# Kernel optimization log

Hardware: AMD Instinct MI355X
Metric: run time of the kernel (lower is better)

## Reference

```python
import jax, jax.numpy as jnp
import numpy as np

D_MODEL = 1024
N_TILES = 16
BATCH = 32768
THRESH = 0.3


def setup_inputs() -> dict:
    key = jax.random.key(0)
    k_x, k_sig, k_w, k_b = jax.random.split(key, 4)
    x = jax.random.normal(k_x, (BATCH, D_MODEL), dtype=jnp.float32)
    # nn.Parameter(torch.randn(n_tiles, d_model) * 0.5)
    signatures_raw = jax.random.normal(k_sig, (N_TILES, D_MODEL), dtype=jnp.float32) * 0.5
    # nn.Linear(d_model, d_model) default init: U(-1/sqrt(fan_in), 1/sqrt(fan_in))
    bound = 1.0 / np.sqrt(D_MODEL)
    W = jax.random.uniform(k_w, (N_TILES, D_MODEL, D_MODEL), dtype=jnp.float32, minval=-bound, maxval=bound)
    b = jax.random.uniform(k_b, (N_TILES, D_MODEL), dtype=jnp.float32, minval=-bound, maxval=bound)
    return {"x": x, "signatures_raw": signatures_raw, "W": W, "b": b}


def _quantize_ternary(s):
    # straight-through ternary: forward value is q, gradient is identity
    q = jnp.where(s > THRESH, 1.0, jnp.where(s < -THRESH, -1.0, 0.0))
    return s + jax.lax.stop_gradient(q - s)


def reference(x, signatures_raw, W, b):
    sigs = _quantize_ternary(signatures_raw)          # [E, D]
    scores = x @ sigs.T                               # [B, E]
    tile_indices = jnp.argmax(scores, axis=-1)        # [B]
    out = jnp.zeros_like(x)
    # fixed small loop over experts: masked combine of per-expert Linear+ReLU
    for e in range(N_TILES):
        y = jax.nn.relu(x @ W[e].T + b[e])            # [B, D]
        out = out + jnp.where((tile_indices == e)[:, None], y, 0.0)
    out = out + x                                     # residual
    return out, tile_indices
```

## Files before the change

### kernel.cpp

```cpp
#include <hip/hip_runtime.h>
#include <hip/hip_bf16.h>

#define BATCH   32768
#define DM      1024
#define NE      16
#define THRESHF 0.3f
#define MARGIN  0.02f

#define CTRL_OFF 131072
#define QBF_OFF  139264
#define PERM_OFF 172032
#define XBF_OFF  319488
#define WB_OFF   67428352ull
#define WS_NEED  (WB_OFF + (size_t)NE * DM * DM * 2)

typedef __attribute__((ext_vector_type(8))) short bf16x8;
typedef __attribute__((ext_vector_type(4))) float f32x4;

#define MFMA16(a, b, c) __builtin_amdgcn_mfma_f32_16x16x32_bf16(a, b, c, 0, 0, 0)

static __device__ __forceinline__ unsigned short f2bf(float f) {
    union { float f; unsigned u; } v; v.f = f;
    unsigned r = (v.u + 0x7FFFu + ((v.u >> 16) & 1u)) >> 16;
    return (unsigned short)r;
}
static __device__ __forceinline__ float bf2f(unsigned short h) {
    union { unsigned u; float f; } v; v.u = ((unsigned)h) << 16;
    return v.f;
}

static __device__ __forceinline__ void gload_lds16(const void* g, void* s) {
    __builtin_amdgcn_global_load_lds(
        (const __attribute__((address_space(1))) void*)g,
        (__attribute__((address_space(3))) void*)s, 16, 0, 0);
}

static __device__ __forceinline__ int tile_base(const unsigned* ctrl, int* tb) {
    int acc = 0;
#pragma unroll
    for (int e = 0; e < NE; ++e) {
        tb[e] = acc;
        acc += (int)((ctrl[e * 16] + 127u) >> 7);
    }
    tb[NE] = acc;
    return acc;
}

__global__ void k_init(const float* __restrict__ sig, unsigned* __restrict__ ctrl,
                       int* __restrict__ perm, unsigned short* __restrict__ Qbf) {
    const int t = blockIdx.x * 256 + threadIdx.x;
    if (t < 544) ctrl[t] = 0;
    if (t < 1024) {
        unsigned pm = 0, mm = 0;
#pragma unroll
        for (int e = 0; e < NE; ++e) {
            float s = sig[e * DM + t];
            pm |= (s > THRESHF ? 1u : 0u) << e;
            mm |= (s < -THRESHF ? 1u : 0u) << e;
        }
        ctrl[1024 + t] = pm | (mm << 16);
    }
    if (t < 9216) ((int4*)perm)[t] = make_int4(0, 0, 0, 0);
    {
        float s = sig[t];
        Qbf[t] = s > THRESHF ? (unsigned short)0x3F80u
                             : (s < -THRESHF ? (unsigned short)0xBF80u : (unsigned short)0u);
    }
}

__global__ __launch_bounds__(256) void k_router(const float* __restrict__ x,
                                                const unsigned short* __restrict__ Qbf,
                                                unsigned* __restrict__ ctrl,
                                                int* __restrict__ idx,
                                                float* __restrict__ outIdx,
                                                unsigned short* __restrict__ Xbf,
                                                int writeXbf) {
    const int t = threadIdx.x, w = t >> 6, l = t & 63;
    const int lc = l & 15, lr = l >> 4;
    const int wid = blockIdx.x * 4 + w;
    const int row0 = wid * 16;
    const unsigned* packT = ctrl + 1024;

    const float* ax = x + (size_t)(row0 + lc) * DM + lr * 8;
    const unsigned short* qx = Qbf + (size_t)lc * DM + lr * 8;
    unsigned short* xb = Xbf + (size_t)(row0 + lc) * DM + lr * 8;

    f32x4 acc = (f32x4){0.f, 0.f, 0.f, 0.f};

    for (int kt = 0; kt < 16; ++kt) {
#pragma unroll
        for (int h = 0; h < 2; ++h) {
            const int ko = kt * 64 + h * 32;
            float4 v0 = *(const float4*)(ax + ko);
            float4 v1 = *(const float4*)(ax + ko + 4);
            bf16x8 q = *(const bf16x8*)(qx + ko);

            float f[8] = {v0.x, v0.y, v0.z, v0.w, v1.x, v1.y, v1.z, v1.w};
            bf16x8 ah, al;
#pragma unroll
            for (int j = 0; j < 8; ++j) {
                unsigned short hi = f2bf(f[j]);
                float r = f[j] - bf2f(hi);
                ah[j] = (short)hi;
                al[j] = (short)f2bf(r);
            }
            if (writeXbf) *(bf16x8*)(xb + ko) = ah;
            acc = MFMA16(ah, q, acc);
            acc = MFMA16(al, q, acc);
        }
    }

    float bv[4]; int bi[4]; float gap[4];
#pragma unroll
    for (int reg = 0; reg < 4; ++reg) {
        float v = acc[reg]; int i = lc; float s = -3.4e38f;
#pragma unroll
        for (int m = 1; m < 16; m <<= 1) {
            float ov = __shfl_xor(v, m, 64);
            int oi = __shfl_xor(i, m, 64);
            float os = __shfl_xor(s, m, 64);
            bool take = (ov > v) || (ov == v && oi < i);
            float loser = take ? v : ov;
            v = take ? ov : v;
            i = take ? oi : i;
            s = fmaxf(fmaxf(s, os), loser);
        }
        bv[reg] = v; bi[reg] = i; gap[reg] = v - s;
    }

    unsigned flagsw = 0;
#pragma unroll
    for (int reg = 0; reg < 4; ++reg)
        flagsw |= (gap[reg] < MARGIN ? 1u : 0u) << reg;

    if (__any(lc == 0 && flagsw != 0)) {
#pragma unroll
        for (int reg = 0; reg < 4; ++reg) {
            for (int g = 0; g < 4; ++g) {
                const unsigned fw = __shfl(flagsw, g * 16, 64);
                if ((fw >> reg) & 1u) {
                    const int row = row0 + g * 4 + reg;
                    const float* xr = x + (size_t)row * DM;
                    float xv[16]; unsigned mk[16];
#pragma unroll
                    for (int k2 = 0; k2 < 16; ++k2) {
                        xv[k2] = xr[k2 * 64 + l];
                        mk[k2] = packT[k2 * 64 + l];
                    }
                    double best = 0.0; int bbi = 0;
                    for (int e = 0; e < 16; ++e) {
                        double a = 0.0;
#pragma unroll
                        for (int k2 = 0; k2 < 16; ++k2) {
                            const int pb = (int)((mk[k2] >> e) & 1u);
                            const int mb = (int)((mk[k2] >> (16 + e)) & 1u);
                            a += pb ? (double)xv[k2] : (mb ? -(double)xv[k2] : 0.0);
                        }
#pragma unroll
                        for (int m = 1; m < 64; m <<= 1) a += __shfl_xor(a, m, 64);
                        if (e == 0 || a > best) { best = a; bbi = e; }
                    }
                    if (lr == g && lc == 0) bi[reg] = bbi;
                }
            }
        }
    }

    if (lc == 0) {
#pragma unroll
        for (int reg = 0; reg < 4; ++reg) {
            const int row = row0 + lr * 4 + reg;
            idx[row] = bi[reg];
            outIdx[row] = (float)bi[reg];
            atomicAdd(&ctrl[bi[reg] * 16], 1u);
        }
    }
}

__global__ __launch_bounds__(256) void k_permconv(const int* __restrict__ idx,
                                                  unsigned* __restrict__ ctrl,
                                                  int* __restrict__ perm,
                                                  const float* __restrict__ W,
                                                  unsigned short* __restrict__ Wb) {
    if (blockIdx.x >= 128) {
        const size_t g = ((size_t)(blockIdx.x - 128) * 256 + threadIdx.x) * 8;
        float4 a = *(const float4*)&W[g];
        float4 b = *(const float4*)&W[g + 4];
        *(ushort4*)&Wb[g]     = make_ushort4(f2bf(a.x), f2bf(a.y), f2bf(a.z), f2bf(a.w));
        *(ushort4*)&Wb[g + 4] = make_ushort4(f2bf(b.x), f2bf(b.y), f2bf(b.z), f2bf(b.w));
        return;
    }
    __shared__ unsigned hcnt[16];
    __shared__ unsigned hbase[16];
    const int t = threadIdx.x;
    const int row = blockIdx.x * 256 + t;
    int tb[NE + 1];
    tile_base(ctrl, tb);
    if (t < 16) hcnt[t] = 0;
    __syncthreads();
    const int e = idx[row];
    const unsigned lrank = atomicAdd(&hcnt[e], 1u);
    __syncthreads();
    if (t < 16) hbase[t] = atomicAdd(&ctrl[256 + t * 16], hcnt[t]);
    __syncthreads();
    perm[tb[e] * 128 + hbase[e] + lrank] = row;
}

__global__ __launch_bounds__(256, 4) void k_gemm(
        const unsigned short* __restrict__ Xbf,
        const unsigned short* __restrict__ Wb,
        const float* __restrict__ bias,
        const int* __restrict__ perm,
        const unsigned* __restrict__ ctrl,
        float* __restrict__ out) {
    __shared__ unsigned short A_lds[3][128 * 32];
    __shared__ unsigned short B_lds[2][128 * 32];

    int tb[NE + 1];
    const int total = tile_base(ctrl, tb);

    int bx, ny;
    {
        const int flat = blockIdx.x;
        const int xcd = flat & 7, s2 = flat >> 3;
        bx = xcd * 34 + (s2 >> 3);
        ny = s2 & 7;
    }
    if (bx >= total) return;
    int e = 0;
    while (e < NE - 1 && tb[e + 1] <= bx) ++e;
    const int valid = (int)ctrl[e * 16] - (bx - tb[e]) * 128;
    const int n0 = ny * 128;

    const int t = threadIdx.x, w = t >> 6, l = t & 63;
    const int wr = w >> 1, wc = w & 1;
    const int lc = l & 15, lr = l >> 4;
    const int hsw = ((t & 3) - ((t >> 3) & 3)) & 3;
    const int ssw = (lr + (lc >> 1)) & 3;

    f32x4 acc[4][4];
#pragma unroll
    for (int m = 0; m < 4; ++m)
#pragma unroll
        for (int n = 0; n < 4; ++n) acc[m][n] = (f32x4){0.f, 0.f, 0.f, 0.f};

    const size_t aRowBase = (size_t)bx * 128;
    const unsigned short* Bg = Wb + ((size_t)e * DM + n0) * DM;

    const int r0 = t >> 2;
    const int prow0 = perm[aRowBase + r0];
    const int prow1 = perm[aRowBase + 64 + r0];
    const unsigned short* a0 = Xbf + (size_t)prow0 * DM + hsw * 8;
    const unsigned short* a1 = Xbf + (size_t)prow1 * DM + hsw * 8;
    const unsigned short* b0 = Bg + (size_t)(t >> 2) * DM + hsw * 8;
    const unsigned short* b1 = Bg + (size_t)(64 + (t >> 2)) * DM + hsw * 8;

    auto STAGE_A = [&](int kt, int buf) {
        const int ko = kt * 32;
        gload_lds16(a0 + ko, &A_lds[buf][(size_t)(w * 64) * 8]);
        gload_lds16(a1 + ko, &A_lds[buf][(size_t)(256 + w * 64) * 8]);
    };
    auto STAGE_B = [&](int kt, int buf) {
        const int ko = kt * 32;
        gload_lds16(b0 + ko, &B_lds[buf][(size_t)(w * 64) * 8]);
        gload_lds16(b1 + ko, &B_lds[buf][(size_t)(256 + w * 64) * 8]);
    };

    STAGE_A(0, 0);
    STAGE_B(0, 0);
    STAGE_A(1, 1);

    const int NT = DM / 32;
    for (int kt = 0; kt < NT; ++kt) {
        if (kt + 1 < NT) asm volatile("s_waitcnt vmcnt(2)" ::: "memory");
        else             asm volatile("s_waitcnt vmcnt(0)" ::: "memory");
        __builtin_amdgcn_sched_barrier(0);
        __builtin_amdgcn_s_barrier();
        __builtin_amdgcn_sched_barrier(0);

        const int ba = kt % 3, bb = kt & 1;
        if (kt + 1 < NT) STAGE_B(kt + 1, bb ^ 1);
        if (kt + 2 < NT) STAGE_A(kt + 2, (ba + 2 >= 3) ? ba - 1 : ba + 2);

        bf16x8 af[4], bf[4];
#pragma unroll
        for (int m = 0; m < 4; ++m)
            af[m] = *(const bf16x8*)&A_lds[ba][(wr * 64 + m * 16 + lc) * 32 + ssw * 8];
#pragma unroll
        for (int n = 0; n < 4; ++n)
            bf[n] = *(const bf16x8*)&B_lds[bb][(wc * 64 + n * 16 + lc) * 32 + ssw * 8];
#pragma unroll
        for (int m = 0; m < 4; ++m)
#pragma unroll
            for (int n = 0; n < 4; ++n)
                acc[m][n] = MFMA16(af[m], bf[n], acc[m][n]);
    }

    float bvv[4];
#pragma unroll
    for (int n = 0; n < 4; ++n) bvv[n] = bias[e * DM + n0 + wc * 64 + n * 16 + lc];

#pragma unroll
    for (int m = 0; m < 4; ++m) {
#pragma unroll
        for (int reg = 0; reg < 4; ++reg) {
            const int rit = wr * 64 + m * 16 + lr * 4 + reg;
            if (rit < valid) {
                const int orow = perm[aRowBase + rit];
                float* op = out + (size_t)orow * DM;
                const unsigned short* xr = Xbf + (size_t)orow * DM;
#pragma unroll
                for (int n = 0; n < 4; ++n) {
                    const int col = n0 + wc * 64 + n * 16 + lc;
                    float v = acc[m][n][reg] + bvv[n];
                    v = v > 0.f ? v : 0.f;
                    op[col] = v + bf2f(xr[col]);
                }
            }
        }
    }
}

__global__ __launch_bounds__(256) void k_gemm_small(
        const float* __restrict__ x, const float* __restrict__ W,
        const float* __restrict__ bias, const int* __restrict__ perm,
        const unsigned* __restrict__ ctrl, float* __restrict__ out) {
    __shared__ unsigned short A_lds[128 * 32];
    __shared__ unsigned short B_lds[128 * 32];
    int tb[NE + 1];
    const int total = tile_base(ctrl, tb);
    int bx, ny;
    {
        const int flat = blockIdx.x;
        const int xcd = flat & 7, s2 = flat >> 3;
        bx = xcd * 34 + (s2 >> 3);
        ny = s2 & 7;
    }
    if (bx >= total) return;
    int e = 0;
    while (e < NE - 1 && tb[e + 1] <= bx) ++e;
    const int valid = (int)ctrl[e * 16] - (bx - tb[e]) * 128;
    const int n0 = ny * 128;
    const int t = threadIdx.x, w = t >> 6, l = t & 63;
    const int wr = w >> 1, wc = w & 1;
    const int lc = l & 15, lr = l >> 4;
    const int hsw = ((t & 3) - ((t >> 3) & 3)) & 3;
    const int ssw = (lr + (lc >> 1)) & 3;

    f32x4 acc[4][4];
#pragma unroll
    for (int m = 0; m < 4; ++m)
#pragma unroll
        for (int n = 0; n < 4; ++n) acc[m][n] = (f32x4){0.f, 0.f, 0.f, 0.f};
    const size_t aRowBase = (size_t)bx * 128;

    for (int kt = 0; kt < DM / 32; ++kt) {
        __syncthreads();
#pragma unroll
        for (int rd = 0; rd < 2; ++rd) {
            const int c = rd * 256 + t;
            const int r = c >> 2;
            const float* wp = W + ((size_t)e * DM + n0 + r) * DM + kt * 32 + hsw * 8;
            float4 q0 = *(const float4*)wp;
            float4 q1 = *(const float4*)(wp + 4);
            *(ushort4*)&B_lds[c * 8]     = make_ushort4(f2bf(q0.x), f2bf(q0.y), f2bf(q0.z), f2bf(q0.w));
            *(ushort4*)&B_lds[c * 8 + 4] = make_ushort4(f2bf(q1.x), f2bf(q1.y), f2bf(q1.z), f2bf(q1.w));
            ushort4 p0 = make_ushort4(0, 0, 0, 0), p1 = p0;
            if (r < valid) {
                const int orow = perm[aRowBase + r];
                const float* xp = x + (size_t)orow * DM + kt * 32 + hsw * 8;
                float4 u0 = *(const float4*)xp;
                float4 u1 = *(const float4*)(xp + 4);
                p0 = make_ushort4(f2bf(u0.x), f2bf(u0.y), f2bf(u0.z), f2bf(u0.w));
                p1 = make_ushort4(f2bf(u1.x), f2bf(u1.y), f2bf(u1.z), f2bf(u1.w));
            }
            *(ushort4*)&A_lds[c * 8]     = p0;
            *(ushort4*)&A_lds[c * 8 + 4] = p1;
        }
        __syncthreads();
        bf16x8 af[4], bf[4];
#pragma unroll
        for (int m = 0; m < 4; ++m)
            af[m] = *(const bf16x8*)&A_lds[(wr * 64 + m * 16 + lc) * 32 + ssw * 8];
#pragma unroll
        for (int n = 0; n < 4; ++n)
            bf[n] = *(const bf16x8*)&B_lds[(wc * 64 + n * 16 + lc) * 32 + ssw * 8];
#pragma unroll
        for (int m = 0; m < 4; ++m)
#pragma unroll
            for (int n = 0; n < 4; ++n)
                acc[m][n] = MFMA16(af[m], bf[n], acc[m][n]);
    }

    float bvv[4];
#pragma unroll
    for (int n = 0; n < 4; ++n) bvv[n] = bias[e * DM + n0 + wc * 64 + n * 16 + lc];
#pragma unroll
    for (int m = 0; m < 4; ++m)
#pragma unroll
        for (int reg = 0; reg < 4; ++reg) {
            const int rit = wr * 64 + m * 16 + lr * 4 + reg;
            if (rit < valid) {
                const int orow = perm[aRowBase + rit];
                const float* xr = x + (size_t)orow * DM;
                float* op = out + (size_t)orow * DM;
#pragma unroll
                for (int n = 0; n < 4; ++n) {
                    const int col = n0 + wc * 64 + n * 16 + lc;
                    float v = acc[m][n][reg] + bvv[n];
                    v = v > 0.f ? v : 0.f;
                    op[col] = v + xr[col];
                }
            }
        }
}

extern "C" void kernel_launch(void* const* d_in, const int* in_sizes, int n_in,
                              void* d_out, int out_size, void* d_ws, size_t ws_size,
                              hipStream_t stream) {
    const float* x    = (const float*)d_in[0];
    const float* sig  = (const float*)d_in[1];
    const float* W    = (const float*)d_in[2];
    const float* bias = (const float*)d_in[3];
    float* out = (float*)d_out;
    float* outIdx = out + (size_t)BATCH * DM;

    char* ws = (char*)d_ws;
    int* idx = (int*)ws;
    unsigned* ctrl = (unsigned*)(ws + CTRL_OFF);
    unsigned short* Qbf = (unsigned short*)(ws + QBF_OFF);
    int* perm = (int*)(ws + PERM_OFF);
    unsigned short* Xbf = (unsigned short*)(ws + XBF_OFF);
    unsigned short* Wb = (unsigned short*)(ws + WB_OFF);

    const bool full = ws_size >= WS_NEED;

    k_init<<<64, 256, 0, stream>>>(sig, ctrl, perm, Qbf);
    k_router<<<512, 256, 0, stream>>>(x, Qbf, ctrl, idx, outIdx, Xbf, full ? 1 : 0);
    k_permconv<<<full ? 8320 : 128, 256, 0, stream>>>(idx, ctrl, perm, W, Wb);
    if (full) {
        k_gemm<<<2176, 256, 0, stream>>>(Xbf, Wb, bias, perm, ctrl, out);
    } else {
        k_gemm_small<<<2176, 256, 0, stream>>>(x, W, bias, perm, ctrl, out);
    }
}
```

Measured before the change: 255.3 us.

## Fuse W conversion into router kernel and triple-buffer B tiles in GEMM

The weight fp32-to-bf16 conversion moves from the permutation kernel into the router kernel as extra blocks, so the bandwidth-bound conversion runs alongside routing and the permutation kernel becomes small. In the GEMM, B is now triple-buffered like A, with one combined stage issuing both loads two iterations ahead and waiting on vmcnt(4). The occupancy hint in launch_bounds is dropped. More LDS per block may lower occupancy, and the router grid is now much larger.

```diff
diff --git a/kernel.cpp b/kernel.cpp
--- a/kernel.cpp
+++ b/kernel.cpp
@@ -68,13 +68,25 @@
     }
 }
 
-__global__ __launch_bounds__(256) void k_router(const float* __restrict__ x,
-                                                const unsigned short* __restrict__ Qbf,
-                                                unsigned* __restrict__ ctrl,
-                                                int* __restrict__ idx,
-                                                float* __restrict__ outIdx,
-                                                unsigned short* __restrict__ Xbf,
-                                                int writeXbf) {
+__global__ __launch_bounds__(256) void k_router_conv(
+        const float* __restrict__ x,
+        const unsigned short* __restrict__ Qbf,
+        unsigned* __restrict__ ctrl,
+        int* __restrict__ idx,
+        float* __restrict__ outIdx,
+        unsigned short* __restrict__ Xbf,
+        const float* __restrict__ W,
+        unsigned short* __restrict__ Wb,
+        int writeXbf) {
+    if (blockIdx.x >= 512) {
+        const size_t g = ((size_t)(blockIdx.x - 512) * 256 + threadIdx.x) * 8;
+        float4 a = *(const float4*)&W[g];
+        float4 b = *(const float4*)&W[g + 4];
+        *(ushort4*)&Wb[g]     = make_ushort4(f2bf(a.x), f2bf(a.y), f2bf(a.z), f2bf(a.w));
+        *(ushort4*)&Wb[g + 4] = make_ushort4(f2bf(b.x), f2bf(b.y), f2bf(b.z), f2bf(b.w));
+        return;
+    }
+
     const int t = threadIdx.x, w = t >> 6, l = t & 63;
     const int lc = l & 15, lr = l >> 4;
     const int wid = blockIdx.x * 4 + w;
@@ -177,19 +189,9 @@
     }
 }
 
-__global__ __launch_bounds__(256) void k_permconv(const int* __restrict__ idx,
-                                                  unsigned* __restrict__ ctrl,
-                                                  int* __restrict__ perm,
-                                                  const float* __restrict__ W,
-                                                  unsigned short* __restrict__ Wb) {
-    if (blockIdx.x >= 128) {
-        const size_t g = ((size_t)(blockIdx.x - 128) * 256 + threadIdx.x) * 8;
-        float4 a = *(const float4*)&W[g];
-        float4 b = *(const float4*)&W[g + 4];
-        *(ushort4*)&Wb[g]     = make_ushort4(f2bf(a.x), f2bf(a.y), f2bf(a.z), f2bf(a.w));
-        *(ushort4*)&Wb[g + 4] = make_ushort4(f2bf(b.x), f2bf(b.y), f2bf(b.z), f2bf(b.w));
-        return;
-    }
+__global__ __launch_bounds__(256) void k_perm(const int* __restrict__ idx,
+                                              unsigned* __restrict__ ctrl,
+                                              int* __restrict__ perm) {
     __shared__ unsigned hcnt[16];
     __shared__ unsigned hbase[16];
     const int t = threadIdx.x;
@@ -206,7 +208,7 @@
     perm[tb[e] * 128 + hbase[e] + lrank] = row;
 }
 
-__global__ __launch_bounds__(256, 4) void k_gemm(
+__global__ __launch_bounds__(256) void k_gemm(
         const unsigned short* __restrict__ Xbf,
         const unsigned short* __restrict__ Wb,
         const float* __restrict__ bias,
@@ -214,7 +216,7 @@
         const unsigned* __restrict__ ctrl,
         float* __restrict__ out) {
     __shared__ unsigned short A_lds[3][128 * 32];
-    __shared__ unsigned short B_lds[2][128 * 32];
+    __shared__ unsigned short B_lds[3][128 * 32];
 
     int tb[NE + 1];
     const int total = tile_base(ctrl, tb);
@@ -255,45 +257,45 @@
     const unsigned short* b0 = Bg + (size_t)(t >> 2) * DM + hsw * 8;
     const unsigned short* b1 = Bg + (size_t)(64 + (t >> 2)) * DM + hsw * 8;
 
-    auto STAGE_A = [&](int kt, int buf) {
+    auto STAGE = [&](int kt, int buf) {
         const int ko = kt * 32;
         gload_lds16(a0 + ko, &A_lds[buf][(size_t)(w * 64) * 8]);
         gload_lds16(a1 + ko, &A_lds[buf][(size_t)(256 + w * 64) * 8]);
-    };
-    auto STAGE_B = [&](int kt, int buf) {
-        const int ko = kt * 32;
         gload_lds16(b0 + ko, &B_lds[buf][(size_t)(w * 64) * 8]);
         gload_lds16(b1 + ko, &B_lds[buf][(size_t)(256 + w * 64) * 8]);
     };
 
-    STAGE_A(0, 0);
-    STAGE_B(0, 0);
-    STAGE_A(1, 1);
+    STAGE(0, 0);
+    STAGE(1, 1);
 
     const int NT = DM / 32;
+    int cur = 0;
     for (int kt = 0; kt < NT; ++kt) {
-        if (kt + 1 < NT) asm volatile("s_waitcnt vmcnt(2)" ::: "memory");
+        if (kt + 1 < NT) asm volatile("s_waitcnt vmcnt(4)" ::: "memory");
         else             asm volatile("s_waitcnt vmcnt(0)" ::: "memory");
         __builtin_amdgcn_sched_barrier(0);
         __builtin_amdgcn_s_barrier();
         __builtin_amdgcn_sched_barrier(0);
 
-        const int ba = kt % 3, bb = kt & 1;
-        if (kt + 1 < NT) STAGE_B(kt + 1, bb ^ 1);
-        if (kt + 2 < NT) STAGE_A(kt + 2, (ba + 2 >= 3) ? ba - 1 : ba + 2);
+        if (kt + 2 < NT) {
+            const int nb = (cur + 2 >= 3) ? cur - 1 : cur + 2;
+            STAGE(kt + 2, nb);
+        }
 
         bf16x8 af[4], bf[4];
 #pragma unroll
         for (int m = 0; m < 4; ++m)
-            af[m] = *(const bf16x8*)&A_lds[ba][(wr * 64 + m * 16 + lc) * 32 + ssw * 8];
+            af[m] = *(const bf16x8*)&A_lds[cur][(wr * 64 + m * 16 + lc) * 32 + ssw * 8];
 #pragma unroll
         for (int n = 0; n < 4; ++n)
-            bf[n] = *(const bf16x8*)&B_lds[bb][(wc * 64 + n * 16 + lc) * 32 + ssw * 8];
+            bf[n] = *(const bf16x8*)&B_lds[cur][(wc * 64 + n * 16 + lc) * 32 + ssw * 8];
 #pragma unroll
         for (int m = 0; m < 4; ++m)
 #pragma unroll
             for (int n = 0; n < 4; ++n)
                 acc[m][n] = MFMA16(af[m], bf[n], acc[m][n]);
+
+        cur = (cur + 1 >= 3) ? 0 : cur + 1;
     }
 
     float bvv[4];
@@ -436,8 +438,9 @@
     const bool full = ws_size >= WS_NEED;
 
     k_init<<<64, 256, 0, stream>>>(sig, ctrl, perm, Qbf);
-    k_router<<<512, 256, 0, stream>>>(x, Qbf, ctrl, idx, outIdx, Xbf, full ? 1 : 0);
-    k_permconv<<<full ? 8320 : 128, 256, 0, stream>>>(idx, ctrl, perm, W, Wb);
+    k_router_conv<<<full ? 8704 : 512, 256, 0, stream>>>(
+        x, Qbf, ctrl, idx, outIdx, Xbf, W, Wb, full ? 1 : 0);
+    k_perm<<<128, 256, 0, stream>>>(idx, ctrl, perm);
     if (full) {
         k_gemm<<<2176, 256, 0, stream>>>(Xbf, Wb, bias, perm, ctrl, out);
     } else {
```

New measurement: 233.9 us. -8.4%, faster.
